# Optimization experiments

Measured on AMD Instinct MI355X. Metric: run time of the kernel, lower is better.

The kernel has to match this reference:

```python
import jax, jax.numpy as jnp
import numpy as np

EPS = 1e-5

def conv1d(x, w, b, pad):
    # x: [B,C_in,S], w: [C_out,C_in,K] -> [B,C_out,S]
    y = jax.lax.conv_general_dilated(x, w, window_strides=(1,), padding=[(pad, pad)],
                                     dimension_numbers=('NCH', 'OIH', 'NCH'))
    return y + b[None, :, None]

def bn(x, gamma, beta, mean, var):
    # inference-mode BatchNorm1d over channel dim of [B,C,S]
    scale = gamma * jax.lax.rsqrt(var + EPS)
    shift = beta - mean * scale
    return x * scale[None, :, None] + shift[None, :, None]

def setup_inputs() -> dict:
    key = jax.random.key(0)
    ks = jax.random.split(key, 16)
    B, S, D, C, K = 32, 2048, 128, 256, 5
    x = jax.random.normal(ks[0], (B, S, D), dtype=jnp.float32)
    start_padding_indices = jax.random.randint(ks[1], (B,), 0, S, dtype=jnp.int64 if jax.config.jax_enable_x64 else jnp.int32)
    def conv_init(k, co, ci, kk):
        fan = ci * kk
        return jax.random.normal(k, (co, ci, kk), dtype=jnp.float32) / np.sqrt(fan)
    W1 = conv_init(ks[2], C, D, K); b1 = jnp.zeros((C,), jnp.float32)
    g1 = jnp.ones((C,), jnp.float32); be1 = jnp.zeros((C,), jnp.float32)
    m1 = jax.random.normal(ks[3], (C,), dtype=jnp.float32) * 0.1
    v1 = jax.random.uniform(ks[4], (C,), dtype=jnp.float32, minval=0.5, maxval=1.5)
    W2 = conv_init(ks[5], C, C, K); b2 = jnp.zeros((C,), jnp.float32)
    g2 = jnp.ones((C,), jnp.float32); be2 = jnp.zeros((C,), jnp.float32)
    m2 = jax.random.normal(ks[6], (C,), dtype=jnp.float32) * 0.1
    v2 = jax.random.uniform(ks[7], (C,), dtype=jnp.float32, minval=0.5, maxval=1.5)
    Wf = conv_init(ks[8], D, C, 1); bf = jnp.zeros((D,), jnp.float32)
    return {"x": x, "start_padding_indices": start_padding_indices,
            "W1": W1, "b1": b1, "g1": g1, "be1": be1, "m1": m1, "v1": v1,
            "W2": W2, "b2": b2, "g2": g2, "be2": be2, "m2": m2, "v2": v2,
            "Wf": Wf, "bf": bf}

def reference(x, start_padding_indices, W1, b1, g1, be1, m1, v1,
              W2, b2, g2, be2, m2, v2, Wf, bf):
    B, S, D = x.shape
    K = W1.shape[-1]
    h = jnp.transpose(x, (0, 2, 1))                      # [B,D,S]
    h = jax.nn.relu(bn(conv1d(h, W1, b1, K // 2), g1, be1, m1, v1))
    h = jax.nn.relu(bn(conv1d(h, W2, b2, K // 2), g2, be2, m2, v2))
    h = conv1d(h, Wf, bf, 0)                             # [B,D,S]
    conv_out = jnp.transpose(h, (0, 2, 1))               # [B,S,D]
    # vectorized masked mean: -1 sentinel -> full length; 0 -> zeros
    lengths = jnp.where(start_padding_indices == -1, S, start_padding_indices)  # [B]
    mask = jnp.arange(S)[None, :] < lengths[:, None]     # [B,S]
    sums = jnp.sum(conv_out * mask[:, :, None].astype(conv_out.dtype), axis=1)  # [B,D]
    denom = jnp.maximum(lengths, 1).astype(conv_out.dtype)[:, None]
    pooled = jnp.where(lengths[:, None] > 0, sums / denom, jnp.zeros_like(sums))
    return pooled
```

## Files before the change

### kernel.cpp

```cpp
#include <hip/hip_runtime.h>

#define S_LEN 2048
#define NBATCH 32

typedef __bf16 bf16x8 __attribute__((ext_vector_type(8)));
typedef float f32x4 __attribute__((ext_vector_type(4)));
typedef unsigned short bf_t;

__device__ __forceinline__ unsigned short f2bf(float f) {
  __bf16 h = (__bf16)f;
  return __builtin_bit_cast(unsigned short, h);
}

#if __has_builtin(__builtin_amdgcn_global_load_lds)
#define USE_GLL 1
#else
#define USE_GLL 0
#endif

__device__ __forceinline__ void load_lds16(const void* g, void* ldsbase) {
#if USE_GLL
  __builtin_amdgcn_global_load_lds(
      (const __attribute__((address_space(1))) unsigned int*)g,
      (__attribute__((address_space(3))) unsigned int*)ldsbase, 16, 0, 0);
#else
  *(int4*)((char*)ldsbase + (threadIdx.x & 63) * 16) =
      *(const int4*)((const char*)g);
#endif
}

#define WAITV8  asm volatile("s_waitcnt vmcnt(8)" ::: "memory")
#define WAITV4  asm volatile("s_waitcnt vmcnt(4)" ::: "memory")
#define WAITV0  asm volatile("s_waitcnt vmcnt(0)" ::: "memory")

__global__ void prep_all(const float* __restrict__ x,
                         const float* __restrict__ W1, const float* __restrict__ W2,
                         const float* __restrict__ Wf,
                         const float* __restrict__ b1, const float* __restrict__ g1,
                         const float* __restrict__ be1, const float* __restrict__ m1,
                         const float* __restrict__ v1,
                         const float* __restrict__ b2, const float* __restrict__ g2,
                         const float* __restrict__ be2, const float* __restrict__ m2,
                         const float* __restrict__ v2,
                         bf_t* __restrict__ xb, bf_t* __restrict__ wf1,
                         bf_t* __restrict__ wf2, bf_t* __restrict__ wff,
                         float* __restrict__ abuf, float* __restrict__ zp) {
  const int bid = blockIdx.x;
  if (bid < 4096) {
    const size_t i = (size_t)bid * 256 + threadIdx.x;
    const float4 a = ((const float4*)x)[2 * i];
    const float4 c = ((const float4*)x)[2 * i + 1];
    ushort4 o0; o0.x = f2bf(a.x); o0.y = f2bf(a.y); o0.z = f2bf(a.z); o0.w = f2bf(a.w);
    ushort4 o1; o1.x = f2bf(c.x); o1.y = f2bf(c.y); o1.z = f2bf(c.z); o1.w = f2bf(c.w);
    ((ushort4*)xb)[2 * i] = o0;
    ((ushort4*)xb)[2 * i + 1] = o1;
  } else if (bid < 6016) {
    const float* w; bf_t* wfm; int idx; int CIN;
    if (bid < 4736) { w = W1; wfm = wf1; idx = (bid - 4096) * 256 + threadIdx.x; CIN = 128; }
    else            { w = W2; wfm = wf2; idx = (bid - 4736) * 256 + threadIdx.x; CIN = 256; }
    const int TAPS = 5;
    const int j = idx & 7;
    const int l = (idx >> 3) & 63;
    const int f = (idx >> 9) & 7;
    const int wr = (idx >> 12) & 1;
    const int tg = idx >> 13;
    const int co = wr * 128 + f * 16 + (l & 15);
    const int cc = tg / (TAPS * 4);
    const int k = (tg / 4) % TAPS;
    const int q = tg & 3;
    const int ci = cc * 128 + q * 32 + (l >> 4) * 8 + j;
    wfm[idx] = f2bf(w[((size_t)co * CIN + ci) * TAPS + k]);
  } else if (bid < 6144) {
    const int idx = (bid - 6016) * 256 + threadIdx.x;
    const int T = 8;
    const int j = idx & 7;
    const int l = (idx >> 3) & 63;
    const int f = (idx >> 9) & 3;
    const int gt = idx >> 11;
    const int t = gt % T;
    const int g = gt / T;
    const int co = g * 64 + f * 16 + (l & 15);
    const int q = t & 3;
    const int cc = t >> 2;
    const int ci = cc * 128 + q * 32 + (l >> 4) * 8 + j;
    wff[idx] = f2bf(Wf[(size_t)co * 256 + ci]);
  } else {
    int c = threadIdx.x;
    if (c < 64) zp[c] = 0.f;
    if (c < 256) {
      float a1 = g1[c] * rsqrtf(v1[c] + 1e-5f);
      abuf[c] = a1;
      abuf[256 + c] = (b1[c] - m1[c]) * a1 + be1[c];
      float a2 = g2[c] * rsqrtf(v2[c] + 1e-5f);
      abuf[512 + c] = a2;
      abuf[768 + c] = (b2[c] - m2[c]) * a2 + be2[c];
    }
  }
}

template <int CIN, int TAPS>
__device__ __forceinline__ void conv_body(
    const bf_t* __restrict__ xin, const bf_t* __restrict__ wfm,
    const float* __restrict__ alpha, const float* __restrict__ bias,
    const float* __restrict__ zp, bf_t* __restrict__ hout) {
  constexpr int HALO = (TAPS - 1) / 2;
  constexpr int P = (CIN / 128) * TAPS * 4;
  constexpr int NKT = P / 2;

  __shared__ char smem[131072];

  const int tid = threadIdx.x;
  const int l = tid & 63;
  const int wv = tid >> 6;
  const int wr = wv >> 2;
  const int wn = wv & 3;
  const int b = blockIdx.x >> 3;
  const int s0 = (blockIdx.x & 7) << 8;
  const int l15 = l & 15;
  const int l4 = l >> 4;
  const int wu16 = (tid - l) * 16;

  f32x4 acc[8][4] = {};

  auto STAGE_A = [&](int jt, int sub) {
    const char* src = (const char*)wfm + (size_t)(2 * jt + sub) * 16384;
    char* dst = smem + (jt & 1) * 32768 + sub * 16384;
    load_lds16(src + tid * 16, dst + wu16);
    load_lds16(src + 8192 + tid * 16, dst + 8192 + wu16);
  };

  auto STAGE_B = [&](int jt, int sub) {
    const int t = 2 * jt + sub;
    const int cc = t / (TAPS * 4);
    const int k = (t >> 2) % TAPS;
    const int q = t & 3;
    char* dst = smem + 65536 + (jt & 1) * 32768 + sub * 16384;
    const int r0 = tid >> 2;
    const int slot = ((r0 & 3) ^ ((r0 >> 2) & 3)) << 4;
    const char* srcb = (const char*)xin +
        ((size_t)b * S_LEN * CIN + cc * 128 + q * 32) * 2 +
        (((tid & 3) * 16) ^ slot);
    {
      const int s = s0 + r0 - HALO + k;
      const char* src = ((unsigned)s < (unsigned)S_LEN)
          ? srcb + (size_t)s * (CIN * 2) : ((const char*)zp + (((tid & 3) * 16) ^ slot));
      load_lds16(src, dst + wu16);
    }
    {
      const int s = s0 + r0 + 128 - HALO + k;
      const char* src = ((unsigned)s < (unsigned)S_LEN)
          ? srcb + (size_t)s * (CIN * 2) : ((const char*)zp + (((tid & 3) * 16) ^ slot));
      load_lds16(src, dst + 8192 + wu16);
    }
  };

  auto LDB = [&](const char* Bb, int sub, int r) -> bf16x8 {
    const int slot = (((r & 3) ^ ((r >> 2) & 3)) << 4);
    return *(const bf16x8*)(Bb + sub * 16384 + r * 64 + ((l4 * 16) ^ slot));
  };

  STAGE_A(0, 0); STAGE_A(0, 1); STAGE_B(0, 0); STAGE_B(0, 1);
  WAITV0;
  STAGE_A(1, 0); STAGE_B(1, 0);
  __builtin_amdgcn_s_barrier();

#pragma unroll 1
  for (int j = 0; j < NKT; ++j) {
    const char* Ab = smem + (j & 1) * 32768;
    const char* Bb = smem + 65536 + (j & 1) * 32768;

    {
      __builtin_amdgcn_s_setprio(1);
      bf16x8 afr[8], bfr[4];
#pragma unroll
      for (int f = 0; f < 8; ++f)
        afr[f] = *(const bf16x8*)(Ab + wr * 8192 + f * 1024 + l * 16);
#pragma unroll
      for (int n = 0; n < 4; ++n)
        bfr[n] = LDB(Bb, 0, wn * 64 + n * 16 + l15);
      if (j + 1 < NKT) { STAGE_B(j + 1, 1); STAGE_A(j + 1, 1); }
#pragma unroll
      for (int f = 0; f < 8; ++f)
#pragma unroll
        for (int n = 0; n < 4; ++n)
          acc[f][n] = __builtin_amdgcn_mfma_f32_16x16x32_bf16(
              afr[f], bfr[n], acc[f][n], 0, 0, 0);
      __builtin_amdgcn_s_setprio(0);
      if (j < NKT - 1) { WAITV8; } else { WAITV0; }
      __builtin_amdgcn_s_barrier();
      __builtin_amdgcn_sched_barrier(0);
    }

    {
      __builtin_amdgcn_s_setprio(1);
      bf16x8 afr[8], bfr[4];
#pragma unroll
      for (int f = 0; f < 8; ++f)
        afr[f] = *(const bf16x8*)(Ab + 16384 + wr * 8192 + f * 1024 + l * 16);
#pragma unroll
      for (int n = 0; n < 4; ++n)
        bfr[n] = LDB(Bb, 1, wn * 64 + n * 16 + l15);
      if (j + 2 < NKT) { STAGE_A(j + 2, 0); STAGE_B(j + 2, 0); }
#pragma unroll
      for (int f = 0; f < 8; ++f)
#pragma unroll
        for (int n = 0; n < 4; ++n)
          acc[f][n] = __builtin_amdgcn_mfma_f32_16x16x32_bf16(
              afr[f], bfr[n], acc[f][n], 0, 0, 0);
      __builtin_amdgcn_s_setprio(0);
      if (j <= NKT - 3) { WAITV8; } else if (j == NKT - 2) { WAITV4; }
      __builtin_amdgcn_s_barrier();
      __builtin_amdgcn_sched_barrier(0);
    }
  }

  WAITV0;
  __syncthreads();
  const int cobase = wr * 128;
#pragma unroll
  for (int f = 0; f < 8; ++f) {
    const int co0 = cobase + f * 16 + l4 * 4;
    const f32x4 al = *(const f32x4*)(alpha + co0);
    const f32x4 bi = *(const f32x4*)(bias + co0);
#pragma unroll
    for (int n = 0; n < 4; ++n) {
      const int sp = wn * 64 + n * 16 + l15;
      ushort4 pk;
      pk.x = f2bf(fmaxf(acc[f][n][0] * al[0] + bi[0], 0.f));
      pk.y = f2bf(fmaxf(acc[f][n][1] * al[1] + bi[1], 0.f));
      pk.z = f2bf(fmaxf(acc[f][n][2] * al[2] + bi[2], 0.f));
      pk.w = f2bf(fmaxf(acc[f][n][3] * al[3] + bi[3], 0.f));
      *(ushort4*)(smem + sp * 512 + ((co0 * 2) ^ ((sp & 7) << 4))) = pk;
    }
  }
  __syncthreads();
  {
    char* hb = (char*)hout + ((size_t)(b * S_LEN + s0) * 256) * 2;
#pragma unroll
    for (int k = 0; k < 16; ++k) {
      const int c = tid + k * 512;
      const int sp = c >> 5;
      const int col = (c & 31) * 16;
      const int4 v = *(const int4*)(smem + sp * 512 + (col ^ ((sp & 7) << 4)));
      *(int4*)(hb + (size_t)sp * 512 + col) = v;
    }
  }
}

__global__ __launch_bounds__(512, 2)
void conv_gemm_L1(const bf_t* __restrict__ xin, const bf_t* __restrict__ wfm,
                  const float* __restrict__ alpha, const float* __restrict__ bias,
                  const float* __restrict__ zp, bf_t* __restrict__ hout) {
  conv_body<128, 5>(xin, wfm, alpha, bias, zp, hout);
}

__global__ __launch_bounds__(512, 2)
void conv_gemm_L2(const bf_t* __restrict__ xin, const bf_t* __restrict__ wfm,
                  const float* __restrict__ alpha, const float* __restrict__ bias,
                  const float* __restrict__ zp, bf_t* __restrict__ hout) {
  conv_body<256, 5>(xin, wfm, alpha, bias, zp, hout);
}

__global__ __launch_bounds__(512, 4)
void conv_pool(const bf_t* __restrict__ xin, const bf_t* __restrict__ wfm,
               const float* __restrict__ bfin, const int* __restrict__ spi,
               float* __restrict__ gpart) {
  constexpr int CIN = 256;
  constexpr int T = 8;

  __shared__ char smem[128 * 256];
  __shared__ float red[4][128];

  const int tid = threadIdx.x;
  const int l = tid & 63;
  const int wv = tid >> 6;
  const int wr = wv >> 2;
  const int wn = wv & 3;
  const int nb = blockIdx.x;
  const int b = nb >> 4;
  const int st = nb & 15;
  const int s0 = st << 7;
  const int l15 = l & 15;
  const int l4 = l >> 4;

  f32x4 acc[4][2] = {};
  const bf_t* wbase = wfm + (size_t)wr * (T * 2048);

  for (int cc = 0; cc < 2; ++cc) {
    const char* src = (const char*)xin + ((size_t)b * S_LEN * CIN + cc * 128) * 2;
    for (int off = tid * 16; off < 128 * 256; off += 512 * 16) {
      const int row = off >> 8;
      const int c = off & 255;
      const int cs = c ^ ((row & 7) << 4);
      void* ldsbase = (void*)(smem + (off - l * 16));
      load_lds16(src + (size_t)(s0 + row) * (CIN * 2) + cs, ldsbase);
    }
    __syncthreads();

#pragma unroll
    for (int q = 0; q < 4; ++q) {
      const int t = cc * 4 + q;
      bf16x8 bfr[2];
#pragma unroll
      for (int fn = 0; fn < 2; ++fn) {
        const int row = wn * 32 + fn * 16 + l15;
        const int cb = q * 64 + l4 * 16;
        bfr[fn] = *(const bf16x8*)(smem + row * 256 + (cb ^ ((row & 7) << 4)));
      }
#pragma unroll
      for (int f = 0; f < 4; ++f) {
        const bf16x8 afr =
            *(const bf16x8*)(wbase + ((size_t)(t * 4 + f) * 64 + l) * 8);
        acc[f][0] = __builtin_amdgcn_mfma_f32_16x16x32_bf16(afr, bfr[0], acc[f][0], 0, 0, 0);
        acc[f][1] = __builtin_amdgcn_mfma_f32_16x16x32_bf16(afr, bfr[1], acc[f][1], 0, 0, 0);
      }
    }
    __syncthreads();
  }

  int len = spi[b];
  if (len < 0) len = S_LEN;

#pragma unroll
  for (int f = 0; f < 4; ++f) {
    const int co0 = wr * 64 + f * 16 + l4 * 4;
    const f32x4 bi = *(const f32x4*)(bfin + co0);
    f32x4 vs = {};
#pragma unroll
    for (int fn = 0; fn < 2; ++fn) {
      const int s = s0 + wn * 32 + fn * 16 + l15;
      const float m = (s < len) ? 1.f : 0.f;
      vs[0] += (acc[f][fn][0] + bi[0]) * m;
      vs[1] += (acc[f][fn][1] + bi[1]) * m;
      vs[2] += (acc[f][fn][2] + bi[2]) * m;
      vs[3] += (acc[f][fn][3] + bi[3]) * m;
    }
#pragma unroll
    for (int d = 1; d < 16; d <<= 1) {
      vs[0] += __shfl_xor(vs[0], d, 64);
      vs[1] += __shfl_xor(vs[1], d, 64);
      vs[2] += __shfl_xor(vs[2], d, 64);
      vs[3] += __shfl_xor(vs[3], d, 64);
    }
    if (l15 == 0) {
      red[wn][co0 + 0] = vs[0];
      red[wn][co0 + 1] = vs[1];
      red[wn][co0 + 2] = vs[2];
      red[wn][co0 + 3] = vs[3];
    }
  }
  __syncthreads();
  if (tid < 128) {
    float p = red[0][tid] + red[1][tid] + red[2][tid] + red[3][tid];
    gpart[((size_t)b * 16 + st) * 128 + tid] = p;
  }
}

__global__ void finalize(const float* __restrict__ gpart, const int* __restrict__ spi,
                         float* __restrict__ out) {
  const int b = blockIdx.x;
  const int d = threadIdx.x;
  float s = 0.f;
#pragma unroll
  for (int t = 0; t < 16; ++t) s += gpart[((size_t)b * 16 + t) * 128 + d];
  int len = spi[b];
  if (len < 0) len = S_LEN;
  float denom = (float)(len < 1 ? 1 : len);
  out[b * 128 + d] = s / denom;
}

extern "C" void kernel_launch(void* const* d_in, const int* in_sizes, int n_in,
                              void* d_out, int out_size, void* d_ws, size_t ws_size,
                              hipStream_t stream) {
  (void)in_sizes; (void)n_in; (void)out_size; (void)ws_size;
  const float* x = (const float*)d_in[0];
  const int* spi = (const int*)d_in[1];
  const float* W1 = (const float*)d_in[2];
  const float* b1 = (const float*)d_in[3];
  const float* g1 = (const float*)d_in[4];
  const float* be1 = (const float*)d_in[5];
  const float* m1 = (const float*)d_in[6];
  const float* v1 = (const float*)d_in[7];
  const float* W2 = (const float*)d_in[8];
  const float* b2 = (const float*)d_in[9];
  const float* g2 = (const float*)d_in[10];
  const float* be2 = (const float*)d_in[11];
  const float* m2 = (const float*)d_in[12];
  const float* v2 = (const float*)d_in[13];
  const float* Wf = (const float*)d_in[14];
  const float* bf_ = (const float*)d_in[15];
  float* out = (float*)d_out;

  char* ws = (char*)d_ws;
  float* zp   = (float*)(ws);
  bf_t* xb    = (bf_t*)(ws + 4096);
  bf_t* h1    = (bf_t*)(ws + 16781312);
  bf_t* h2    = (bf_t*)(ws + 50335744);
  bf_t* wf1   = (bf_t*)(ws + 83890176);
  bf_t* wf2   = (bf_t*)(ws + 84217856);
  bf_t* wff   = (bf_t*)(ws + 84873216);
  float* abuf = (float*)(ws + 84938752);
  float* gpart= (float*)(ws + 84942848);

  prep_all<<<6145, 256, 0, stream>>>(x, W1, W2, Wf,
                                     b1, g1, be1, m1, v1,
                                     b2, g2, be2, m2, v2,
                                     xb, wf1, wf2, wff, abuf, zp);
  conv_gemm_L1<<<256, 512, 0, stream>>>(xb, wf1, abuf, abuf + 256, zp, h1);
  conv_gemm_L2<<<256, 512, 0, stream>>>(h1, wf2, abuf + 512, abuf + 768, zp, h2);
  conv_pool<<<512, 512, 0, stream>>>(h2, wff, bf_, spi, gpart);
  finalize<<<32, 128, 0, stream>>>(gpart, spi, out);
}
```

Measured before the change: 97.33 us.

## Load conv weight fragments straight to registers and halve LDS footprint

The A (weight) operand no longer goes through LDS: each wave loads its weight fragments from global memory directly into registers, double-buffered across the two sub-steps. Only the activation tile is staged in LDS, which cuts shared memory per block from 128KB to 64KB. The epilogue writes output in two 128-row halves so it fits the smaller buffer, and the vmcnt wait counts are retuned for the new mix of outstanding loads. The likely goal is higher occupancy and less LDS traffic, at the cost of extra VGPRs and weight loads that each wave issues from global/L2 on its own.

```diff
diff --git a/kernel.cpp b/kernel.cpp
--- a/kernel.cpp
+++ b/kernel.cpp
@@ -29,8 +29,8 @@
 #endif
 }
 
-#define WAITV8  asm volatile("s_waitcnt vmcnt(8)" ::: "memory")
-#define WAITV4  asm volatile("s_waitcnt vmcnt(4)" ::: "memory")
+#define WAITV10 asm volatile("s_waitcnt vmcnt(10)" ::: "memory")
+#define WAITV2  asm volatile("s_waitcnt vmcnt(2)" ::: "memory")
 #define WAITV0  asm volatile("s_waitcnt vmcnt(0)" ::: "memory")
 
 __global__ void prep_all(const float* __restrict__ x,
@@ -107,7 +107,7 @@
   constexpr int P = (CIN / 128) * TAPS * 4;
   constexpr int NKT = P / 2;
 
-  __shared__ char smem[131072];
+  __shared__ char smem[65536];
 
   const int tid = threadIdx.x;
   const int l = tid & 63;
@@ -121,20 +121,15 @@
   const int wu16 = (tid - l) * 16;
 
   f32x4 acc[8][4] = {};
-
-  auto STAGE_A = [&](int jt, int sub) {
-    const char* src = (const char*)wfm + (size_t)(2 * jt + sub) * 16384;
-    char* dst = smem + (jt & 1) * 32768 + sub * 16384;
-    load_lds16(src + tid * 16, dst + wu16);
-    load_lds16(src + 8192 + tid * 16, dst + 8192 + wu16);
-  };
+  bf16x8 afrA[8], afrB[8];
+  const char* aw = (const char*)wfm + wr * 8192 + l * 16;
 
   auto STAGE_B = [&](int jt, int sub) {
     const int t = 2 * jt + sub;
     const int cc = t / (TAPS * 4);
     const int k = (t >> 2) % TAPS;
     const int q = t & 3;
-    char* dst = smem + 65536 + (jt & 1) * 32768 + sub * 16384;
+    char* dst = smem + (jt & 1) * 32768 + sub * 16384;
     const int r0 = tid >> 2;
     const int slot = ((r0 & 3) ^ ((r0 >> 2) & 3)) << 4;
     const char* srcb = (const char*)xin +
@@ -159,56 +154,59 @@
     return *(const bf16x8*)(Bb + sub * 16384 + r * 64 + ((l4 * 16) ^ slot));
   };
 
-  STAGE_A(0, 0); STAGE_A(0, 1); STAGE_B(0, 0); STAGE_B(0, 1);
-  WAITV0;
-  STAGE_A(1, 0); STAGE_B(1, 0);
+#pragma unroll
+  for (int f = 0; f < 8; ++f)
+    afrA[f] = *(const bf16x8*)(aw + f * 1024);
+  STAGE_B(0, 0); STAGE_B(0, 1); STAGE_B(1, 0);
+  WAITV2;
   __builtin_amdgcn_s_barrier();
 
 #pragma unroll 1
   for (int j = 0; j < NKT; ++j) {
-    const char* Ab = smem + (j & 1) * 32768;
-    const char* Bb = smem + 65536 + (j & 1) * 32768;
+    const char* Bb = smem + (j & 1) * 32768;
 
     {
       __builtin_amdgcn_s_setprio(1);
-      bf16x8 afr[8], bfr[4];
-#pragma unroll
-      for (int f = 0; f < 8; ++f)
-        afr[f] = *(const bf16x8*)(Ab + wr * 8192 + f * 1024 + l * 16);
+      bf16x8 bfr[4];
 #pragma unroll
       for (int n = 0; n < 4; ++n)
         bfr[n] = LDB(Bb, 0, wn * 64 + n * 16 + l15);
-      if (j + 1 < NKT) { STAGE_B(j + 1, 1); STAGE_A(j + 1, 1); }
+#pragma unroll
+      for (int f = 0; f < 8; ++f)
+        afrB[f] = *(const bf16x8*)(aw + (size_t)(2 * j + 1) * 16384 + f * 1024);
+      if (j + 1 < NKT) STAGE_B(j + 1, 1);
 #pragma unroll
       for (int f = 0; f < 8; ++f)
 #pragma unroll
         for (int n = 0; n < 4; ++n)
           acc[f][n] = __builtin_amdgcn_mfma_f32_16x16x32_bf16(
-              afr[f], bfr[n], acc[f][n], 0, 0, 0);
+              afrA[f], bfr[n], acc[f][n], 0, 0, 0);
       __builtin_amdgcn_s_setprio(0);
-      if (j < NKT - 1) { WAITV8; } else { WAITV0; }
+      WAITV10;
       __builtin_amdgcn_s_barrier();
       __builtin_amdgcn_sched_barrier(0);
     }
 
     {
       __builtin_amdgcn_s_setprio(1);
-      bf16x8 afr[8], bfr[4];
-#pragma unroll
-      for (int f = 0; f < 8; ++f)
-        afr[f] = *(const bf16x8*)(Ab + 16384 + wr * 8192 + f * 1024 + l * 16);
+      bf16x8 bfr[4];
 #pragma unroll
       for (int n = 0; n < 4; ++n)
         bfr[n] = LDB(Bb, 1, wn * 64 + n * 16 + l15);
-      if (j + 2 < NKT) { STAGE_A(j + 2, 0); STAGE_B(j + 2, 0); }
+      if (j + 1 < NKT) {
+#pragma unroll
+        for (int f = 0; f < 8; ++f)
+          afrA[f] = *(const bf16x8*)(aw + (size_t)(2 * j + 2) * 16384 + f * 1024);
+      }
+      if (j + 2 < NKT) STAGE_B(j + 2, 0);
 #pragma unroll
       for (int f = 0; f < 8; ++f)
 #pragma unroll
         for (int n = 0; n < 4; ++n)
           acc[f][n] = __builtin_amdgcn_mfma_f32_16x16x32_bf16(
-              afr[f], bfr[n], acc[f][n], 0, 0, 0);
+              afrB[f], bfr[n], acc[f][n], 0, 0, 0);
       __builtin_amdgcn_s_setprio(0);
-      if (j <= NKT - 3) { WAITV8; } else if (j == NKT - 2) { WAITV4; }
+      if (j < NKT - 1) { WAITV10; } else { WAITV0; }
       __builtin_amdgcn_s_barrier();
       __builtin_amdgcn_sched_barrier(0);
     }
@@ -218,32 +216,39 @@
   __syncthreads();
   const int cobase = wr * 128;
 #pragma unroll
-  for (int f = 0; f < 8; ++f) {
-    const int co0 = cobase + f * 16 + l4 * 4;
-    const f32x4 al = *(const f32x4*)(alpha + co0);
-    const f32x4 bi = *(const f32x4*)(bias + co0);
-#pragma unroll
-    for (int n = 0; n < 4; ++n) {
-      const int sp = wn * 64 + n * 16 + l15;
-      ushort4 pk;
-      pk.x = f2bf(fmaxf(acc[f][n][0] * al[0] + bi[0], 0.f));
-      pk.y = f2bf(fmaxf(acc[f][n][1] * al[1] + bi[1], 0.f));
-      pk.z = f2bf(fmaxf(acc[f][n][2] * al[2] + bi[2], 0.f));
-      pk.w = f2bf(fmaxf(acc[f][n][3] * al[3] + bi[3], 0.f));
-      *(ushort4*)(smem + sp * 512 + ((co0 * 2) ^ ((sp & 7) << 4))) = pk;
-    }
-  }
-  __syncthreads();
-  {
-    char* hb = (char*)hout + ((size_t)(b * S_LEN + s0) * 256) * 2;
-#pragma unroll
-    for (int k = 0; k < 16; ++k) {
-      const int c = tid + k * 512;
-      const int sp = c >> 5;
-      const int col = (c & 31) * 16;
-      const int4 v = *(const int4*)(smem + sp * 512 + (col ^ ((sp & 7) << 4)));
-      *(int4*)(hb + (size_t)sp * 512 + col) = v;
-    }
+  for (int h = 0; h < 2; ++h) {
+    if ((wn >> 1) == h) {
+#pragma unroll
+      for (int f = 0; f < 8; ++f) {
+        const int co0 = cobase + f * 16 + l4 * 4;
+        const f32x4 al = *(const f32x4*)(alpha + co0);
+        const f32x4 bi = *(const f32x4*)(bias + co0);
+#pragma unroll
+        for (int n = 0; n < 4; ++n) {
+          const int sp = wn * 64 + n * 16 + l15;
+          const int spl = sp & 127;
+          ushort4 pk;
+          pk.x = f2bf(fmaxf(acc[f][n][0] * al[0] + bi[0], 0.f));
+          pk.y = f2bf(fmaxf(acc[f][n][1] * al[1] + bi[1], 0.f));
+          pk.z = f2bf(fmaxf(acc[f][n][2] * al[2] + bi[2], 0.f));
+          pk.w = f2bf(fmaxf(acc[f][n][3] * al[3] + bi[3], 0.f));
+          *(ushort4*)(smem + spl * 512 + ((co0 * 2) ^ ((sp & 7) << 4))) = pk;
+        }
+      }
+    }
+    __syncthreads();
+    {
+      char* hb = (char*)hout + ((size_t)(b * S_LEN + s0 + h * 128) * 256) * 2;
+#pragma unroll
+      for (int k = 0; k < 8; ++k) {
+        const int c = tid + k * 512;
+        const int spl = c >> 5;
+        const int col = (c & 31) * 16;
+        const int4 v = *(const int4*)(smem + spl * 512 + (col ^ ((spl & 7) << 4)));
+        *(int4*)(hb + (size_t)spl * 512 + col) = v;
+      }
+    }
+    __syncthreads();
   }
 }
 
```

After: 111.5 us. 1.15x slower.

## Pool before final 1x1 conv and fuse masked pooling into layer-2 epilogue

Applied to the files above, without the earlier changes.

Uses linearity of the final pointwise conv to swap it with the masked mean. Layer 2 now reduces its ReLU outputs over the valid sequence positions in its epilogue and writes per-tile partial sums instead of the full h2 activation. A small matvec kernel then applies Wf and the bias to the pooled vector. This removes the h2 write/read round trip, the conv_pool GEMM, the Wf repack and one launch. In exchange, the last projection runs in fp32 on a tiny per-batch matvec, so rounding differs slightly from the previous bf16 path.

```diff
diff --git a/kernel.cpp b/kernel.cpp
--- a/kernel.cpp
+++ b/kernel.cpp
@@ -35,7 +35,6 @@
 
 __global__ void prep_all(const float* __restrict__ x,
                          const float* __restrict__ W1, const float* __restrict__ W2,
-                         const float* __restrict__ Wf,
                          const float* __restrict__ b1, const float* __restrict__ g1,
                          const float* __restrict__ be1, const float* __restrict__ m1,
                          const float* __restrict__ v1,
@@ -43,7 +42,7 @@
                          const float* __restrict__ be2, const float* __restrict__ m2,
                          const float* __restrict__ v2,
                          bf_t* __restrict__ xb, bf_t* __restrict__ wf1,
-                         bf_t* __restrict__ wf2, bf_t* __restrict__ wff,
+                         bf_t* __restrict__ wf2,
                          float* __restrict__ abuf, float* __restrict__ zp) {
   const int bid = blockIdx.x;
   if (bid < 4096) {
@@ -70,20 +69,6 @@
     const int q = tg & 3;
     const int ci = cc * 128 + q * 32 + (l >> 4) * 8 + j;
     wfm[idx] = f2bf(w[((size_t)co * CIN + ci) * TAPS + k]);
-  } else if (bid < 6144) {
-    const int idx = (bid - 6016) * 256 + threadIdx.x;
-    const int T = 8;
-    const int j = idx & 7;
-    const int l = (idx >> 3) & 63;
-    const int f = (idx >> 9) & 3;
-    const int gt = idx >> 11;
-    const int t = gt % T;
-    const int g = gt / T;
-    const int co = g * 64 + f * 16 + (l & 15);
-    const int q = t & 3;
-    const int cc = t >> 2;
-    const int ci = cc * 128 + q * 32 + (l >> 4) * 8 + j;
-    wff[idx] = f2bf(Wf[(size_t)co * 256 + ci]);
   } else {
     int c = threadIdx.x;
     if (c < 64) zp[c] = 0.f;
@@ -98,11 +83,12 @@
   }
 }
 
-template <int CIN, int TAPS>
+template <int CIN, int TAPS, bool POOL>
 __device__ __forceinline__ void conv_body(
     const bf_t* __restrict__ xin, const bf_t* __restrict__ wfm,
     const float* __restrict__ alpha, const float* __restrict__ bias,
-    const float* __restrict__ zp, bf_t* __restrict__ hout) {
+    const float* __restrict__ zp, bf_t* __restrict__ hout,
+    const int* __restrict__ spi, float* __restrict__ hpart) {
   constexpr int HALO = (TAPS - 1) / 2;
   constexpr int P = (CIN / 128) * TAPS * 4;
   constexpr int NKT = P / 2;
@@ -216,25 +202,26 @@
 
   WAITV0;
   __syncthreads();
-  const int cobase = wr * 128;
-#pragma unroll
-  for (int f = 0; f < 8; ++f) {
-    const int co0 = cobase + f * 16 + l4 * 4;
-    const f32x4 al = *(const f32x4*)(alpha + co0);
-    const f32x4 bi = *(const f32x4*)(bias + co0);
-#pragma unroll
-    for (int n = 0; n < 4; ++n) {
-      const int sp = wn * 64 + n * 16 + l15;
-      ushort4 pk;
-      pk.x = f2bf(fmaxf(acc[f][n][0] * al[0] + bi[0], 0.f));
-      pk.y = f2bf(fmaxf(acc[f][n][1] * al[1] + bi[1], 0.f));
-      pk.z = f2bf(fmaxf(acc[f][n][2] * al[2] + bi[2], 0.f));
-      pk.w = f2bf(fmaxf(acc[f][n][3] * al[3] + bi[3], 0.f));
-      *(ushort4*)(smem + sp * 512 + ((co0 * 2) ^ ((sp & 7) << 4))) = pk;
-    }
-  }
-  __syncthreads();
-  {
+
+  if constexpr (!POOL) {
+    const int cobase = wr * 128;
+#pragma unroll
+    for (int f = 0; f < 8; ++f) {
+      const int co0 = cobase + f * 16 + l4 * 4;
+      const f32x4 al = *(const f32x4*)(alpha + co0);
+      const f32x4 bi = *(const f32x4*)(bias + co0);
+#pragma unroll
+      for (int n = 0; n < 4; ++n) {
+        const int sp = wn * 64 + n * 16 + l15;
+        ushort4 pk;
+        pk.x = f2bf(fmaxf(acc[f][n][0] * al[0] + bi[0], 0.f));
+        pk.y = f2bf(fmaxf(acc[f][n][1] * al[1] + bi[1], 0.f));
+        pk.z = f2bf(fmaxf(acc[f][n][2] * al[2] + bi[2], 0.f));
+        pk.w = f2bf(fmaxf(acc[f][n][3] * al[3] + bi[3], 0.f));
+        *(ushort4*)(smem + sp * 512 + ((co0 * 2) ^ ((sp & 7) << 4))) = pk;
+      }
+    }
+    __syncthreads();
     char* hb = (char*)hout + ((size_t)(b * S_LEN + s0) * 256) * 2;
 #pragma unroll
     for (int k = 0; k < 16; ++k) {
@@ -244,6 +231,52 @@
       const int4 v = *(const int4*)(smem + sp * 512 + (col ^ ((sp & 7) << 4)));
       *(int4*)(hb + (size_t)sp * 512 + col) = v;
     }
+  } else {
+    float* red = (float*)smem;
+    int len = spi[b];
+    if (len < 0) len = S_LEN;
+    const int cobase = wr * 128;
+#pragma unroll
+    for (int f = 0; f < 8; ++f) {
+      const int co0 = cobase + f * 16 + l4 * 4;
+      const f32x4 al = *(const f32x4*)(alpha + co0);
+      const f32x4 bi = *(const f32x4*)(bias + co0);
+      f32x4 vs = {};
+#pragma unroll
+      for (int n = 0; n < 4; ++n) {
+        const int s = s0 + wn * 64 + n * 16 + l15;
+        const float m = (s < len) ? 1.f : 0.f;
+        vs[0] += fmaxf(acc[f][n][0] * al[0] + bi[0], 0.f) * m;
+        vs[1] += fmaxf(acc[f][n][1] * al[1] + bi[1], 0.f) * m;
+        vs[2] += fmaxf(acc[f][n][2] * al[2] + bi[2], 0.f) * m;
+        vs[3] += fmaxf(acc[f][n][3] * al[3] + bi[3], 0.f) * m;
+      }
+#pragma unroll
+      for (int d = 1; d < 16; d <<= 1) {
+        vs[0] += __shfl_xor(vs[0], d, 64);
+        vs[1] += __shfl_xor(vs[1], d, 64);
+        vs[2] += __shfl_xor(vs[2], d, 64);
+        vs[3] += __shfl_xor(vs[3], d, 64);
+      }
+      if (l15 == 0) {
+        float* rp = red + ((wv * 8 + f) * 4 + l4) * 4;
+        rp[0] = vs[0]; rp[1] = vs[1]; rp[2] = vs[2]; rp[3] = vs[3];
+      }
+    }
+    __syncthreads();
+    if (tid < 256) {
+      const int co = tid;
+      const int wrc = co >> 7;
+      const int fc = (co >> 4) & 7;
+      const int l4c = (co >> 2) & 3;
+      const int jc = co & 3;
+      float s = 0.f;
+#pragma unroll
+      for (int w = 0; w < 4; ++w)
+        s += red[(((wrc * 4 + w) * 8 + fc) * 4 + l4c) * 4 + jc];
+      const int pt = blockIdx.x & 7;
+      hpart[((size_t)b * 8 + pt) * 256 + co] = s;
+    }
   }
 }
 
@@ -251,122 +284,40 @@
 void conv_gemm_L1(const bf_t* __restrict__ xin, const bf_t* __restrict__ wfm,
                   const float* __restrict__ alpha, const float* __restrict__ bias,
                   const float* __restrict__ zp, bf_t* __restrict__ hout) {
-  conv_body<128, 5>(xin, wfm, alpha, bias, zp, hout);
+  conv_body<128, 5, false>(xin, wfm, alpha, bias, zp, hout, nullptr, nullptr);
 }
 
 __global__ __launch_bounds__(512, 2)
 void conv_gemm_L2(const bf_t* __restrict__ xin, const bf_t* __restrict__ wfm,
                   const float* __restrict__ alpha, const float* __restrict__ bias,
-                  const float* __restrict__ zp, bf_t* __restrict__ hout) {
-  conv_body<256, 5>(xin, wfm, alpha, bias, zp, hout);
-}
-
-__global__ __launch_bounds__(512, 4)
-void conv_pool(const bf_t* __restrict__ xin, const bf_t* __restrict__ wfm,
-               const float* __restrict__ bfin, const int* __restrict__ spi,
-               float* __restrict__ gpart) {
-  constexpr int CIN = 256;
-  constexpr int T = 8;
-
-  __shared__ char smem[128 * 256];
-  __shared__ float red[4][128];
-
+                  const float* __restrict__ zp, const int* __restrict__ spi,
+                  float* __restrict__ hpart) {
+  conv_body<256, 5, true>(xin, wfm, alpha, bias, zp, nullptr, spi, hpart);
+}
+
+__global__ void pool_matvec(const float* __restrict__ hpart,
+                            const float* __restrict__ Wf,
+                            const float* __restrict__ bf_,
+                            const int* __restrict__ spi,
+                            float* __restrict__ out) {
+  __shared__ float S[256];
+  const int b = blockIdx.x;
   const int tid = threadIdx.x;
-  const int l = tid & 63;
-  const int wv = tid >> 6;
-  const int wr = wv >> 2;
-  const int wn = wv & 3;
-  const int nb = blockIdx.x;
-  const int b = nb >> 4;
-  const int st = nb & 15;
-  const int s0 = st << 7;
-  const int l15 = l & 15;
-  const int l4 = l >> 4;
-
-  f32x4 acc[4][2] = {};
-  const bf_t* wbase = wfm + (size_t)wr * (T * 2048);
-
-  for (int cc = 0; cc < 2; ++cc) {
-    const char* src = (const char*)xin + ((size_t)b * S_LEN * CIN + cc * 128) * 2;
-    for (int off = tid * 16; off < 128 * 256; off += 512 * 16) {
-      const int row = off >> 8;
-      const int c = off & 255;
-      const int cs = c ^ ((row & 7) << 4);
-      void* ldsbase = (void*)(smem + (off - l * 16));
-      load_lds16(src + (size_t)(s0 + row) * (CIN * 2) + cs, ldsbase);
-    }
-    __syncthreads();
-
-#pragma unroll
-    for (int q = 0; q < 4; ++q) {
-      const int t = cc * 4 + q;
-      bf16x8 bfr[2];
-#pragma unroll
-      for (int fn = 0; fn < 2; ++fn) {
-        const int row = wn * 32 + fn * 16 + l15;
-        const int cb = q * 64 + l4 * 16;
-        bfr[fn] = *(const bf16x8*)(smem + row * 256 + (cb ^ ((row & 7) << 4)));
-      }
-#pragma unroll
-      for (int f = 0; f < 4; ++f) {
-        const bf16x8 afr =
-            *(const bf16x8*)(wbase + ((size_t)(t * 4 + f) * 64 + l) * 8);
-        acc[f][0] = __builtin_amdgcn_mfma_f32_16x16x32_bf16(afr, bfr[0], acc[f][0], 0, 0, 0);
-        acc[f][1] = __builtin_amdgcn_mfma_f32_16x16x32_bf16(afr, bfr[1], acc[f][1], 0, 0, 0);
-      }
-    }
-    __syncthreads();
+  for (int c = tid; c < 256; c += 128) {
+    float s = 0.f;
+#pragma unroll
+    for (int pt = 0; pt < 8; ++pt) s += hpart[((size_t)b * 8 + pt) * 256 + c];
+    S[c] = s;
   }
-
+  __syncthreads();
   int len = spi[b];
   if (len < 0) len = S_LEN;
-
-#pragma unroll
-  for (int f = 0; f < 4; ++f) {
-    const int co0 = wr * 64 + f * 16 + l4 * 4;
-    const f32x4 bi = *(const f32x4*)(bfin + co0);
-    f32x4 vs = {};
-#pragma unroll
-    for (int fn = 0; fn < 2; ++fn) {
-      const int s = s0 + wn * 32 + fn * 16 + l15;
-      const float m = (s < len) ? 1.f : 0.f;
-      vs[0] += (acc[f][fn][0] + bi[0]) * m;
-      vs[1] += (acc[f][fn][1] + bi[1]) * m;
-      vs[2] += (acc[f][fn][2] + bi[2]) * m;
-      vs[3] += (acc[f][fn][3] + bi[3]) * m;
-    }
-#pragma unroll
-    for (int d = 1; d < 16; d <<= 1) {
-      vs[0] += __shfl_xor(vs[0], d, 64);
-      vs[1] += __shfl_xor(vs[1], d, 64);
-      vs[2] += __shfl_xor(vs[2], d, 64);
-      vs[3] += __shfl_xor(vs[3], d, 64);
-    }
-    if (l15 == 0) {
-      red[wn][co0 + 0] = vs[0];
-      red[wn][co0 + 1] = vs[1];
-      red[wn][co0 + 2] = vs[2];
-      red[wn][co0 + 3] = vs[3];
-    }
-  }
-  __syncthreads();
-  if (tid < 128) {
-    float p = red[0][tid] + red[1][tid] + red[2][tid] + red[3][tid];
-    gpart[((size_t)b * 16 + st) * 128 + tid] = p;
-  }
-}
-
-__global__ void finalize(const float* __restrict__ gpart, const int* __restrict__ spi,
-                         float* __restrict__ out) {
-  const int b = blockIdx.x;
-  const int d = threadIdx.x;
-  float s = 0.f;
-#pragma unroll
-  for (int t = 0; t < 16; ++t) s += gpart[((size_t)b * 16 + t) * 128 + d];
-  int len = spi[b];
-  if (len < 0) len = S_LEN;
-  float denom = (float)(len < 1 ? 1 : len);
-  out[b * 128 + d] = s / denom;
+  float a = 0.f;
+  const float* wrow = Wf + (size_t)tid * 256;
+  for (int c = 0; c < 256; ++c) a += wrow[c] * S[c];
+  float res = 0.f;
+  if (len > 0) res = (a + (float)len * bf_[tid]) / (float)len;
+  out[b * 128 + tid] = res;
 }
 
 extern "C" void kernel_launch(void* const* d_in, const int* in_sizes, int n_in,
@@ -395,19 +346,17 @@
   float* zp   = (float*)(ws);
   bf_t* xb    = (bf_t*)(ws + 4096);
   bf_t* h1    = (bf_t*)(ws + 16781312);
-  bf_t* h2    = (bf_t*)(ws + 50335744);
   bf_t* wf1   = (bf_t*)(ws + 83890176);
   bf_t* wf2   = (bf_t*)(ws + 84217856);
-  bf_t* wff   = (bf_t*)(ws + 84873216);
   float* abuf = (float*)(ws + 84938752);
-  float* gpart= (float*)(ws + 84942848);
-
-  prep_all<<<6145, 256, 0, stream>>>(x, W1, W2, Wf,
+  float* hpart= (float*)(ws + 84942848);
+
+  prep_all<<<6017, 256, 0, stream>>>(x, W1, W2,
                                      b1, g1, be1, m1, v1,
                                      b2, g2, be2, m2, v2,
-                                     xb, wf1, wf2, wff, abuf, zp);
+                                     xb, wf1, wf2, abuf, zp);
   conv_gemm_L1<<<256, 512, 0, stream>>>(xb, wf1, abuf, abuf + 256, zp, h1);
-  conv_gemm_L2<<<256, 512, 0, stream>>>(h1, wf2, abuf + 512, abuf + 768, zp, h2);
-  conv_pool<<<512, 512, 0, stream>>>(h2, wff, bf_, spi, gpart);
-  finalize<<<32, 128, 0, stream>>>(gpart, spi, out);
-}
+  conv_gemm_L2<<<256, 512, 0, stream>>>(h1, wf2, abuf + 512, abuf + 768, zp,
+                                        spi, hpart);
+  pool_matvec<<<32, 128, 0, stream>>>(hpart, Wf, bf_, spi, out);
+}
```

Measured after the change: 88.25 us, median of 2. -9.3%, faster.
